# Kernel tuning notes

Measured on AMD Instinct MI355X. Metric: run time of the kernel, lower is better.

The kernel has to match this reference:

```python
import jax, jax.numpy as jnp
import numpy as np

B, N, C, H = 8, 1024, 768, 12
D = C // H
HID = 4 * C
MAX_TEXT_LEN = 512
LN_EPS = 1e-5


def _ln(x, g, b):
    mu = jnp.mean(x, axis=-1, keepdims=True)
    var = jnp.mean(jnp.square(x - mu), axis=-1, keepdims=True)
    return (x - mu) * jax.lax.rsqrt(var + LN_EPS) * g + b


def _mlp(x, w1, b1, w2, b2):
    h = jax.nn.gelu(x @ w1.T + b1, approximate=False)
    return h @ w2.T + b2


def setup_inputs() -> dict:
    key = jax.random.key(0)
    ks = jax.random.split(key, 16)
    s = 0.02
    return {
        "x": jax.random.normal(ks[0], (B, N, C), jnp.float32),
        "mask": jax.random.randint(ks[1], (B, N), 0, 2).astype(bool),
        "rel_bias": jax.random.normal(ks[2], (H, N, N), jnp.float32) * s,
        "w_qkv": jax.random.normal(ks[3], (3 * C, C), jnp.float32) * s,
        "q_bias": jnp.zeros((C,), jnp.float32),
        "v_bias": jnp.zeros((C,), jnp.float32),
        "w_proj": jax.random.normal(ks[4], (C, C), jnp.float32) * s,
        "b_proj": jnp.zeros((C,), jnp.float32),
        "ln1_g": jnp.ones((C,), jnp.float32),
        "ln1_b": jnp.zeros((C,), jnp.float32),
        "ln2t_g": jnp.ones((C,), jnp.float32),
        "ln2t_b": jnp.zeros((C,), jnp.float32),
        "ln2i_g": jnp.ones((C,), jnp.float32),
        "ln2i_b": jnp.zeros((C,), jnp.float32),
        "w1t": jax.random.normal(ks[5], (HID, C), jnp.float32) * s,
        "b1t": jnp.zeros((HID,), jnp.float32),
        "w2t": jax.random.normal(ks[6], (C, HID), jnp.float32) * s,
        "b2t": jnp.zeros((C,), jnp.float32),
        "w1i": jax.random.normal(ks[7], (HID, C), jnp.float32) * s,
        "b1i": jnp.zeros((HID,), jnp.float32),
        "w2i": jax.random.normal(ks[8], (C, HID), jnp.float32) * s,
        "b2i": jnp.zeros((C,), jnp.float32),
        "gamma1": jnp.full((C,), 0.1, jnp.float32),
        "gamma2": jnp.full((C,), 0.1, jnp.float32),
    }


def reference(x, mask, rel_bias, w_qkv, q_bias, v_bias, w_proj, b_proj,
              ln1_g, ln1_b, ln2t_g, ln2t_b, ln2i_g, ln2i_b,
              w1t, b1t, w2t, b2t, w1i, b1i, w2i, b2i, gamma1, gamma2):
    # ---- attention branch ----
    h = _ln(x, ln1_g, ln1_b)
    qkv_bias = jnp.concatenate([q_bias, jnp.zeros_like(v_bias), v_bias])
    qkv = h @ w_qkv.T + qkv_bias                      # [B,N,3C]
    qkv = qkv.reshape(B, N, 3, H, D).transpose(2, 0, 3, 1, 4)  # [3,B,H,N,D]
    q, k, v = qkv[0], qkv[1], qkv[2]
    q = q * (D ** -0.5)
    attn = jnp.einsum('bhnd,bhmd->bhnm',
                      q.astype(jnp.float32), k.astype(jnp.float32))
    attn = attn + rel_bias[None]                      # [B,H,N,N]
    attn = jnp.where(mask[:, None, None, :], attn, -jnp.inf)
    attn = jax.nn.softmax(attn, axis=-1).astype(x.dtype)
    out = jnp.einsum('bhnm,bhmd->bhnd', attn, v)
    out = out.transpose(0, 2, 1, 3).reshape(B, N, C)
    out = out @ w_proj.T + b_proj
    x = x + gamma1 * out
    # ---- dual-branch layer-scaled MLP (mlp_vl is None path) ----
    xt = x[:, :MAX_TEXT_LEN]
    xi = x[:, MAX_TEXT_LEN:]
    xt = xt + gamma2 * _mlp(_ln(xt, ln2t_g, ln2t_b), w1t, b1t, w2t, b2t)
    xi = xi + gamma2 * _mlp(_ln(xi, ln2i_g, ln2i_b), w1i, b1i, w2i, b2i)
    return jnp.concatenate([xt, xi], axis=1)
```

## Files before the change

### kernel.cpp

```cpp
#include <hip/hip_runtime.h>
#include <hip/hip_bf16.h>
#include <math.h>

#define B_    8
#define N_TOK 1024
#define C_    768
#define H_    12
#define D_    64
#define HID_  3072

typedef __attribute__((ext_vector_type(4)))  float f32x4;
typedef __attribute__((ext_vector_type(16))) float f32x16;
typedef __attribute__((ext_vector_type(8)))  short s16x8;
typedef __attribute__((ext_vector_type(4)))  unsigned short u16x4;

static __device__ __forceinline__ unsigned short f2bf(float x){
  union { __hip_bfloat16 h; unsigned short u; } cv;
  cv.h = __float2bfloat16(x);
  return cv.u;
}
static __device__ __forceinline__ float bf2f(unsigned short u){
  return __uint_as_float(((unsigned)u) << 16);
}

#define GLOAD_LDS16(gp, lp) \
  __builtin_amdgcn_global_load_lds((const __attribute__((address_space(1))) unsigned int*)(gp), \
                                   (__attribute__((address_space(3))) unsigned int*)(lp), 16, 0, 0)

__global__ __launch_bounds__(256) void k_cvtall(
    const float* __restrict__ wq,  const float* __restrict__ wp,
    const float* __restrict__ w1t, const float* __restrict__ w2t,
    const float* __restrict__ w1i, const float* __restrict__ w2i,
    const float* __restrict__ bias,
    unsigned short* __restrict__ dq,  unsigned short* __restrict__ dp,
    unsigned short* __restrict__ d1t, unsigned short* __restrict__ d2t,
    unsigned short* __restrict__ d1i, unsigned short* __restrict__ d2i,
    unsigned short* __restrict__ db)
{
  int i = blockIdx.x * 256 + threadIdx.x;
  const float* src; unsigned short* dst; int o;
  if      (i <  442368){ src = wq;  dst = dq;  o = i; }
  else if (i <  589824){ src = wp;  dst = dp;  o = i -  442368; }
  else if (i < 1179648){ src = w1t; dst = d1t; o = i -  589824; }
  else if (i < 1769472){ src = w2t; dst = d2t; o = i - 1179648; }
  else if (i < 2359296){ src = w1i; dst = d1i; o = i - 1769472; }
  else if (i < 2949120){ src = w2i; dst = d2i; o = i - 2359296; }
  else                 { src = bias;dst = db;  o = i - 2949120; }
  float4 v = ((const float4*)src)[o];
  u16x4 r;
  r.x = f2bf(v.x); r.y = f2bf(v.y); r.z = f2bf(v.z); r.w = f2bf(v.w);
  *(u16x4*)(dst + (size_t)o*4) = r;
}

__global__ __launch_bounds__(256) void k_ln1(const float* __restrict__ x,
                                             const float* __restrict__ g,
                                             const float* __restrict__ bta,
                                             unsigned short* __restrict__ out){
  int row  = blockIdx.x*4 + (threadIdx.x >> 6);
  int lane = threadIdx.x & 63;
  const float* xr = x + (size_t)row*C_;
  float v[12]; float s = 0.f;
  #pragma unroll
  for (int i=0;i<12;i++){ v[i] = xr[lane + i*64]; s += v[i]; }
  #pragma unroll
  for (int m=1;m<64;m<<=1) s += __shfl_xor(s, m);
  float mu = s * (1.f/768.f);
  float vs = 0.f;
  #pragma unroll
  for (int i=0;i<12;i++){ float d = v[i]-mu; vs += d*d; }
  #pragma unroll
  for (int m=1;m<64;m<<=1) vs += __shfl_xor(vs, m);
  float rs = rsqrtf(vs*(1.f/768.f) + 1e-5f);
  unsigned short* orow = out + (size_t)row*C_;
  #pragma unroll
  for (int i=0;i<12;i++){ int c = lane + i*64; orow[c] = f2bf((v[i]-mu)*rs*g[c] + bta[c]); }
}

__global__ __launch_bounds__(256) void k_ln2(const float* __restrict__ xmid,
                                             const float* __restrict__ gt, const float* __restrict__ bt,
                                             const float* __restrict__ gi, const float* __restrict__ bi,
                                             unsigned short* __restrict__ outc){
  int row  = blockIdx.x*4 + (threadIdx.x >> 6);
  int lane = threadIdx.x & 63;
  int bb = row >> 10, n = row & 1023;
  const float* G = (n < 512) ? gt : gi;
  const float* Bb = (n < 512) ? bt : bi;
  int crow = (n < 512) ? (bb*512 + n) : (4096 + bb*512 + (n - 512));
  const float* xr = xmid + (size_t)row*C_;
  float v[12]; float s = 0.f;
  #pragma unroll
  for (int i=0;i<12;i++){ v[i] = xr[lane + i*64]; s += v[i]; }
  #pragma unroll
  for (int m=1;m<64;m<<=1) s += __shfl_xor(s, m);
  float mu = s * (1.f/768.f);
  float vs = 0.f;
  #pragma unroll
  for (int i=0;i<12;i++){ float d = v[i]-mu; vs += d*d; }
  #pragma unroll
  for (int m=1;m<64;m<<=1) vs += __shfl_xor(vs, m);
  float rs = rsqrtf(vs*(1.f/768.f) + 1e-5f);
  unsigned short* orow = outc + (size_t)crow*C_;
  #pragma unroll
  for (int i=0;i<12;i++){ int c = lane + i*64; orow[c] = f2bf((v[i]-mu)*rs*G[c] + Bb[c]); }
}

template<int MODE>
__global__ __launch_bounds__(256, 3) void k_gemm2(
    const unsigned short* __restrict__ A,
    const unsigned short* __restrict__ Bw0,
    const unsigned short* __restrict__ Bw1,
    int K,
    const float* __restrict__ bias0,
    const float* __restrict__ bias1,
    const float* __restrict__ qb2,
    const float* __restrict__ resid,
    const float* __restrict__ gamma,
    unsigned short* __restrict__ out_bf,
    float* __restrict__ out_f)
{
  __shared__ __align__(16) char smem[49152];
  const int tid = threadIdx.x;
  const int lane = tid & 63, w = tid >> 6;
  const int wr = w >> 1, wc = w & 1;
  const int g16 = lane >> 4, c16 = lane & 15;

  const int gx = gridDim.x;
  const int nwg = gx * gridDim.y;
  const int flat = blockIdx.y * gx + blockIdx.x;
  const int nid = (flat & 7) * (nwg >> 3) + (flat >> 3);
  const int bx = nid % gx, by = nid / gx;
  const int z = blockIdx.z;
  const int row0 = bx*128, col0 = by*128;

  const unsigned short* Ap = A;
  const unsigned short* Bp = Bw0;
  const float* bias = bias0;
  if (MODE == 2 || MODE == 3){
    if (z){ Ap = A + (size_t)4096*K; Bp = Bw1; bias = bias1; }
  }
  const char* Abase = (const char*)Ap;
  const char* Bbase = (const char*)Bp;
  const size_t rowbytes = (size_t)K*2;
  const int KT2 = K >> 5;

  auto stage = [&](int h, int slot_idx){
    char* slot = smem + slot_idx*16384;
    size_t kb = (size_t)h*64;
    #pragma unroll
    for (int it = 0; it < 2; it++){
      int L = it*4096 + tid*16;
      int r = L >> 6, cb = L & 63;
      int scb = cb ^ ((r & 6) << 3);
      GLOAD_LDS16(Abase + (size_t)(row0 + r)*rowbytes + kb + scb, slot + L);
    }
    #pragma unroll
    for (int it = 0; it < 2; it++){
      int L = it*4096 + tid*16;
      int r = L >> 6, cb = L & 63;
      int scb = cb ^ ((r & 6) << 3);
      GLOAD_LDS16(Bbase + (size_t)(col0 + r)*rowbytes + kb + scb, slot + 8192 + L);
    }
  };

  stage(0, 0); stage(1, 1);
  asm volatile("s_waitcnt vmcnt(4)" ::: "memory");
  __builtin_amdgcn_s_barrier();

  f32x4 acc[4][4] = {};
  int sh = 2;
  int sc_ = 0;
  for (int h = 0; h < KT2; h++){
    if (h + 2 < KT2){
      stage(h + 2, sh);
      sh = (sh == 2) ? 0 : sh + 1;
    }
    char* slot = smem + sc_*16384;
    sc_ = (sc_ == 2) ? 0 : sc_ + 1;
    s16x8 af[4], bf[4];
    #pragma unroll
    for (int i = 0; i < 4; i++){
      int ra = wr*64 + i*16 + c16;
      af[i] = *(const s16x8*)(slot + ra*64 + ((g16*16) ^ ((ra & 6) << 3)));
      int rb = wc*64 + i*16 + c16;
      bf[i] = *(const s16x8*)(slot + 8192 + rb*64 + ((g16*16) ^ ((rb & 6) << 3)));
    }
    __builtin_amdgcn_s_setprio(1);
    #pragma unroll
    for (int mi = 0; mi < 4; mi++)
      #pragma unroll
      for (int ni = 0; ni < 4; ni++)
        acc[mi][ni] = __builtin_amdgcn_mfma_f32_16x16x32_bf16(af[mi], bf[ni], acc[mi][ni], 0, 0, 0);
    __builtin_amdgcn_s_setprio(0);
    if (h + 1 < KT2){
      if (h + 2 < KT2) asm volatile("s_waitcnt vmcnt(4)" ::: "memory");
      else             asm volatile("s_waitcnt vmcnt(0)" ::: "memory");
      __builtin_amdgcn_s_barrier();
    }
  }

  #pragma unroll
  for (int mi = 0; mi < 4; mi++){
    int mbase = row0 + wr*64 + mi*16 + g16*4;
    #pragma unroll
    for (int ni = 0; ni < 4; ni++){
      int j = col0 + wc*64 + ni*16 + c16;
      f32x4 a = acc[mi][ni];
      if (MODE == 0){
        int which = (j >= 1536) ? 2 : (j >= 768 ? 1 : 0);
        int cj = j - which*768;
        float bs = (which == 0) ? bias0[cj] : (which == 2 ? qb2[cj] : 0.f);
        int head = cj >> 6, d = cj & 63;
        #pragma unroll
        for (int r = 0; r < 4; r++){
          int mm = mbase + r;
          int bb = mm >> 10, n = mm & 1023;
          float val = a[r] + bs;
          if (which == 0) val *= 0.125f;
          out_bf[((((size_t)which*B_ + bb)*H_ + head)*N_TOK + n)*D_ + d] = f2bf(val);
        }
      } else if (MODE == 1){
        float gm = gamma[j], bs = bias[j];
        #pragma unroll
        for (int r = 0; r < 4; r++){
          size_t idx = (size_t)(mbase + r)*C_ + j;
          out_f[idx] = resid[idx] + gm*(a[r] + bs);
        }
      } else if (MODE == 2){
        float bs = bias[j];
        unsigned short* outp = out_bf + (size_t)z*4096*HID_;
        #pragma unroll
        for (int r = 0; r < 4; r++){
          float t = a[r] + bs;
          outp[(size_t)(mbase + r)*HID_ + j] = f2bf(0.5f*t*(1.f + erff(t*0.70710678118654752f)));
        }
      } else {
        float gm = gamma[j], bs = bias[j];
        #pragma unroll
        for (int r = 0; r < 4; r++){
          int mm = mbase + r;
          int bb = mm >> 9, n = (mm & 511) + (z ? 512 : 0);
          size_t idx = ((size_t)bb*N_TOK + n)*C_ + j;
          out_f[idx] = resid[idx] + gm*(a[r] + bs);
        }
      }
    }
  }
}

__global__ __launch_bounds__(256, 3) void k_attn(
    const unsigned short* __restrict__ qb,
    const unsigned short* __restrict__ kb,
    const unsigned short* __restrict__ vb,
    const unsigned short* __restrict__ bias_bf,
    const int* __restrict__ mask,
    unsigned short* __restrict__ outb)
{
  __shared__ __align__(16) char smem[45056];
  char* Vt0 = smem;
  char* Vt1 = smem + 8192;
  char* Ks  = smem + 16384;
  char* Bs  = smem + 24576;
  float* maskf = (float*)(smem + 40960);
  char* Oep = smem;

  int wg = blockIdx.x;
  int x = wg & 7, rest = wg >> 3;
  int qt = rest & 7, gl = rest >> 3;
  int g = gl*8 + x;
  int h = g % 12, bb = g / 12;

  const int tid = threadIdx.x, lane = tid & 63, w = tid >> 6;
  const int l31 = lane & 31, h5 = lane >> 5;
  const size_t bh = (size_t)bb*H_ + h;
  const char* qp = (const char*)(qb + bh*N_TOK*D_);
  const char* kp = (const char*)(kb + bh*N_TOK*D_);
  const unsigned short* vp = vb + bh*N_TOK*D_;
  const char* bp = (const char*)(bias_bf + (size_t)h*N_TOK*N_TOK);
  const int q0 = qt*128;
  const int qrow = q0 + w*32 + l31;
  const int qr = w*32 + l31;

  #pragma unroll
  for (int it = 0; it < 2; it++){
    int L = it*4096 + tid*16; int r = L >> 7, cb = L & 127;
    GLOAD_LDS16(kp + (size_t)r*128 + (cb ^ ((r & 7) << 4)), Ks + L);
  }
  #pragma unroll
  for (int it = 0; it < 4; it++){
    int L = it*4096 + tid*16; int r = L >> 7, cb = L & 127;
    GLOAD_LDS16(bp + (size_t)(q0 + r)*2048 + (cb ^ ((r & 7) << 4)), Bs + L);
  }
  unsigned short vv[16];
  #pragma unroll
  for (int j = 0; j < 16; j++) vv[j] = vp[(size_t)(w*16 + j)*D_ + lane];
  {
    int4 m4 = *(const int4*)(mask + bb*N_TOK + tid*4);
    float4 f4;
    f4.x = m4.x ? 0.f : -1e30f; f4.y = m4.y ? 0.f : -1e30f;
    f4.z = m4.z ? 0.f : -1e30f; f4.w = m4.w ? 0.f : -1e30f;
    *(float4*)(maskf + tid*4) = f4;
  }
  s16x8 qf[4];
  #pragma unroll
  for (int t = 0; t < 4; t++)
    qf[t] = *(const s16x8*)(qp + (size_t)qrow*128 + t*32 + h5*16);
  #pragma unroll
  for (int i = 0; i < 2; i++){
    s16x8 pk;
    #pragma unroll
    for (int e = 0; e < 8; e++) pk[e] = (short)vv[i*8 + e];
    *(s16x8*)(Vt0 + lane*128 + ((w*32 + i*16) ^ ((lane & 7) << 4))) = pk;
  }
  __syncthreads();

  f32x16 oacc[2] = {};
  float lrow = 0.f;

  for (int t = 0; t < 16; t++){
    const int kt = t*64;
    char* Vbuf = (t & 1) ? Vt1 : Vt0;
    char* Vnxt = (t & 1) ? Vt0 : Vt1;

    s16x8 kfr[2][4];
    #pragma unroll
    for (int ck = 0; ck < 2; ck++)
      #pragma unroll
      for (int tt = 0; tt < 4; tt++)
        kfr[ck][tt] = *(const s16x8*)(Ks + (ck*32 + l31)*128 + ((tt*32 + h5*16) ^ ((l31 & 7) << 4)));
    u16x4 bv[2][4];
    #pragma unroll
    for (int ck = 0; ck < 2; ck++)
      #pragma unroll
      for (int rq = 0; rq < 4; rq++){
        int off = ck*64 + rq*16 + h5*8;
        bv[ck][rq] = *(const u16x4*)(Bs + qr*128 + (off ^ ((qr & 7) << 4)));
      }
    __syncthreads();

    if (t < 15){
      #pragma unroll
      for (int it = 0; it < 2; it++){
        int L = it*4096 + tid*16; int r = L >> 7, cb = L & 127;
        GLOAD_LDS16(kp + (size_t)(kt + 64 + r)*128 + (cb ^ ((r & 7) << 4)), Ks + L);
      }
      #pragma unroll
      for (int it = 0; it < 4; it++){
        int L = it*4096 + tid*16; int r = L >> 7, cb = L & 127;
        GLOAD_LDS16(bp + (size_t)(q0 + r)*2048 + (size_t)(kt + 64)*2 + (cb ^ ((r & 7) << 4)), Bs + L);
      }
      #pragma unroll
      for (int j = 0; j < 16; j++)
        vv[j] = vp[(size_t)(kt + 64 + w*16 + j)*D_ + lane];
    }

    f32x16 sacc[2] = {};
    __builtin_amdgcn_s_setprio(1);
    #pragma unroll
    for (int tt = 0; tt < 4; tt++){
      sacc[0] = __builtin_amdgcn_mfma_f32_32x32x16_bf16(kfr[0][tt], qf[tt], sacc[0], 0, 0, 0);
      sacc[1] = __builtin_amdgcn_mfma_f32_32x32x16_bf16(kfr[1][tt], qf[tt], sacc[1], 0, 0, 0);
    }
    __builtin_amdgcn_s_setprio(0);

    float sv[2][16];
    float ps = 0.f;
    #pragma unroll
    for (int ck = 0; ck < 2; ck++){
      #pragma unroll
      for (int r = 0; r < 16; r++){
        int kk = ck*32 + (r & 3) + 8*(r >> 2) + 4*h5;
        float p = __expf(sacc[ck][r] + bf2f(bv[ck][r >> 2][r & 3]) + maskf[kt + kk]);
        sv[ck][r] = p;
        ps += p;
      }
    }
    lrow += ps;

    #pragma unroll
    for (int ck = 0; ck < 2; ck++){
      #pragma unroll
      for (int kh = 0; kh < 2; kh++){
        unsigned wA, wB, wC, wD;
        asm("v_cvt_pk_bf16_f32 %0, %1, %2" : "=v"(wA) : "v"(sv[ck][kh*8+0]), "v"(sv[ck][kh*8+1]));
        asm("v_cvt_pk_bf16_f32 %0, %1, %2" : "=v"(wB) : "v"(sv[ck][kh*8+2]), "v"(sv[ck][kh*8+3]));
        asm("v_cvt_pk_bf16_f32 %0, %1, %2" : "=v"(wC) : "v"(sv[ck][kh*8+4]), "v"(sv[ck][kh*8+5]));
        asm("v_cvt_pk_bf16_f32 %0, %1, %2" : "=v"(wD) : "v"(sv[ck][kh*8+6]), "v"(sv[ck][kh*8+7]));
        unsigned tA = (unsigned)__shfl_xor((int)wA, 32);
        unsigned tB = (unsigned)__shfl_xor((int)wB, 32);
        unsigned tC = (unsigned)__shfl_xor((int)wC, 32);
        unsigned tD = (unsigned)__shfl_xor((int)wD, 32);
        union { unsigned u[4]; s16x8 v; } pu;
        pu.u[0] = h5 ? tC : wA;
        pu.u[1] = h5 ? tD : wB;
        pu.u[2] = h5 ? wC : tA;
        pu.u[3] = h5 ? wD : tB;
        __builtin_amdgcn_s_setprio(1);
        #pragma unroll
        for (int dt = 0; dt < 2; dt++){
          int d = dt*32 + l31;
          s16x8 vf = *(const s16x8*)(Vbuf + d*128 + ((ck*64 + kh*32 + h5*16) ^ ((d & 7) << 4)));
          oacc[dt] = __builtin_amdgcn_mfma_f32_32x32x16_bf16(vf, pu.v, oacc[dt], 0, 0, 0);
        }
        __builtin_amdgcn_s_setprio(0);
      }
    }

    if (t < 15){
      #pragma unroll
      for (int i = 0; i < 2; i++){
        s16x8 pk;
        #pragma unroll
        for (int e = 0; e < 8; e++) pk[e] = (short)vv[i*8 + e];
        *(s16x8*)(Vnxt + lane*128 + ((w*32 + i*16) ^ ((lane & 7) << 4))) = pk;
      }
    }
    __syncthreads();
  }

  lrow += __shfl_xor(lrow, 32);
  float inv = 1.f / lrow;
  char* Ow = Oep + w*8192;
  #pragma unroll
  for (int dt = 0; dt < 2; dt++)
    #pragma unroll
    for (int r = 0; r < 16; r++){
      int d = dt*32 + (r & 3) + 8*(r >> 2) + 4*h5;
      *(float*)(Ow + l31*256 + ((d*4) ^ ((l31 & 7) << 4))) = oacc[dt][r] * inv;
    }
  int q2 = lane >> 1, dh = lane & 1;
  float of[32];
  #pragma unroll
  for (int i = 0; i < 8; i++){
    f32x4 v4 = *(const f32x4*)(Ow + q2*256 + ((dh*128 + i*16) ^ ((q2 & 7) << 4)));
    of[i*4+0] = v4[0]; of[i*4+1] = v4[1]; of[i*4+2] = v4[2]; of[i*4+3] = v4[3];
  }
  unsigned short* orow = outb + ((size_t)bb*N_TOK + q0 + w*32 + q2)*C_ + h*64 + dh*32;
  #pragma unroll
  for (int i = 0; i < 4; i++){
    s16x8 ob;
    #pragma unroll
    for (int e = 0; e < 8; e++) ob[e] = (short)f2bf(of[i*8+e]);
    *(s16x8*)(orow + i*8) = ob;
  }
}

extern "C" void kernel_launch(void* const* d_in, const int* in_sizes, int n_in,
                              void* d_out, int out_size, void* d_ws, size_t ws_size,
                              hipStream_t stream) {
  const float* x      = (const float*)d_in[0];
  const int*   mask   = (const int*)  d_in[1];
  const float* relb   = (const float*)d_in[2];
  const float* w_qkv  = (const float*)d_in[3];
  const float* q_bias = (const float*)d_in[4];
  const float* v_bias = (const float*)d_in[5];
  const float* w_proj = (const float*)d_in[6];
  const float* b_proj = (const float*)d_in[7];
  const float* ln1_g  = (const float*)d_in[8];
  const float* ln1_b  = (const float*)d_in[9];
  const float* ln2t_g = (const float*)d_in[10];
  const float* ln2t_b = (const float*)d_in[11];
  const float* ln2i_g = (const float*)d_in[12];
  const float* ln2i_b = (const float*)d_in[13];
  const float* w1t    = (const float*)d_in[14];
  const float* b1t    = (const float*)d_in[15];
  const float* w2t    = (const float*)d_in[16];
  const float* b2t    = (const float*)d_in[17];
  const float* w1i    = (const float*)d_in[18];
  const float* b1i    = (const float*)d_in[19];
  const float* w2i    = (const float*)d_in[20];
  const float* b2i    = (const float*)d_in[21];
  const float* gamma1 = (const float*)d_in[22];
  const float* gamma2 = (const float*)d_in[23];
  float* out = (float*)d_out;
  char* ws = (char*)d_ws;

  size_t off = 0;
  auto nxt = [&](size_t b){ size_t r = off; off += (b + 255) & ~(size_t)255; return r; };
  unsigned short* wq_bf  = (unsigned short*)(ws + nxt((size_t)3*C_*C_*2));
  unsigned short* wp_bf  = (unsigned short*)(ws + nxt((size_t)C_*C_*2));
  unsigned short* w1t_bf = (unsigned short*)(ws + nxt((size_t)HID_*C_*2));
  unsigned short* w2t_bf = (unsigned short*)(ws + nxt((size_t)HID_*C_*2));
  unsigned short* w1i_bf = (unsigned short*)(ws + nxt((size_t)HID_*C_*2));
  unsigned short* w2i_bf = (unsigned short*)(ws + nxt((size_t)HID_*C_*2));
  unsigned short* hln    = (unsigned short*)(ws + nxt((size_t)B_*N_TOK*C_*2));
  unsigned short* qkv    = (unsigned short*)(ws + nxt((size_t)3*B_*N_TOK*C_*2));
  unsigned short* attno  = (unsigned short*)(ws + nxt((size_t)B_*N_TOK*C_*2));
  float*          xmid   = (float*)(ws + nxt((size_t)B_*N_TOK*C_*4));
  unsigned short* ln2c   = hln;
  unsigned short* hidden = qkv;
  unsigned short* bias_bf = (unsigned short*)xmid;

  k_cvtall<<<dim3(23808), 256, 0, stream>>>(w_qkv, w_proj, w1t, w2t, w1i, w2i, relb,
                                            wq_bf, wp_bf, w1t_bf, w2t_bf, w1i_bf, w2i_bf, bias_bf);

  k_ln1<<<dim3(B_*N_TOK/4), 256, 0, stream>>>(x, ln1_g, ln1_b, hln);

  k_gemm2<0><<<dim3(64, 18, 1), 256, 0, stream>>>(hln, wq_bf, nullptr, C_,
                                                  q_bias, nullptr, v_bias,
                                                  nullptr, nullptr, qkv, nullptr);

  const size_t qsz = (size_t)B_*H_*N_TOK*D_;
  k_attn<<<dim3(768), 256, 0, stream>>>(qkv, qkv + qsz, qkv + 2*qsz, bias_bf, mask, attno);

  k_gemm2<1><<<dim3(64, 6, 1), 256, 0, stream>>>(attno, wp_bf, nullptr, C_,
                                                 b_proj, nullptr, nullptr,
                                                 x, gamma1, nullptr, xmid);

  k_ln2<<<dim3(B_*N_TOK/4), 256, 0, stream>>>(xmid, ln2t_g, ln2t_b, ln2i_g, ln2i_b, ln2c);

  k_gemm2<2><<<dim3(32, 24, 2), 256, 0, stream>>>(ln2c, w1t_bf, w1i_bf, C_,
                                                  b1t, b1i, nullptr,
                                                  nullptr, nullptr, hidden, nullptr);

  k_gemm2<3><<<dim3(32, 6, 2), 256, 0, stream>>>(hidden, w2t_bf, w2i_bf, HID_,
                                                 b2t, b2i, nullptr,
                                                 xmid, gamma2, nullptr, out);
}
```

Baseline: 322.4 us.

## Use 32x32 MFMA in GEMMs and read fp32 rel-bias directly in attention

```diff
diff --git a/kernel.cpp b/kernel.cpp
--- a/kernel.cpp
+++ b/kernel.cpp
@@ -19,9 +19,6 @@
   cv.h = __float2bfloat16(x);
   return cv.u;
 }
-static __device__ __forceinline__ float bf2f(unsigned short u){
-  return __uint_as_float(((unsigned)u) << 16);
-}
 
 #define GLOAD_LDS16(gp, lp) \
   __builtin_amdgcn_global_load_lds((const __attribute__((address_space(1))) unsigned int*)(gp), \
@@ -31,11 +28,9 @@
     const float* __restrict__ wq,  const float* __restrict__ wp,
     const float* __restrict__ w1t, const float* __restrict__ w2t,
     const float* __restrict__ w1i, const float* __restrict__ w2i,
-    const float* __restrict__ bias,
     unsigned short* __restrict__ dq,  unsigned short* __restrict__ dp,
     unsigned short* __restrict__ d1t, unsigned short* __restrict__ d2t,
-    unsigned short* __restrict__ d1i, unsigned short* __restrict__ d2i,
-    unsigned short* __restrict__ db)
+    unsigned short* __restrict__ d1i, unsigned short* __restrict__ d2i)
 {
   int i = blockIdx.x * 256 + threadIdx.x;
   const float* src; unsigned short* dst; int o;
@@ -44,8 +39,7 @@
   else if (i < 1179648){ src = w1t; dst = d1t; o = i -  589824; }
   else if (i < 1769472){ src = w2t; dst = d2t; o = i - 1179648; }
   else if (i < 2359296){ src = w1i; dst = d1i; o = i - 1769472; }
-  else if (i < 2949120){ src = w2i; dst = d2i; o = i - 2359296; }
-  else                 { src = bias;dst = db;  o = i - 2949120; }
+  else                 { src = w2i; dst = d2i; o = i - 2359296; }
   float4 v = ((const float4*)src)[o];
   u16x4 r;
   r.x = f2bf(v.x); r.y = f2bf(v.y); r.z = f2bf(v.z); r.w = f2bf(v.w);
@@ -122,7 +116,7 @@
   const int tid = threadIdx.x;
   const int lane = tid & 63, w = tid >> 6;
   const int wr = w >> 1, wc = w & 1;
-  const int g16 = lane >> 4, c16 = lane & 15;
+  const int l31 = lane & 31, h5 = lane >> 5;
 
   const int gx = gridDim.x;
   const int nwg = gx * gridDim.y;
@@ -166,7 +160,7 @@
   asm volatile("s_waitcnt vmcnt(4)" ::: "memory");
   __builtin_amdgcn_s_barrier();
 
-  f32x4 acc[4][4] = {};
+  f32x16 acc[2][2] = {};
   int sh = 2;
   int sc_ = 0;
   for (int h = 0; h < KT2; h++){
@@ -176,20 +170,29 @@
     }
     char* slot = smem + sc_*16384;
     sc_ = (sc_ == 2) ? 0 : sc_ + 1;
-    s16x8 af[4], bf[4];
-    #pragma unroll
-    for (int i = 0; i < 4; i++){
-      int ra = wr*64 + i*16 + c16;
-      af[i] = *(const s16x8*)(slot + ra*64 + ((g16*16) ^ ((ra & 6) << 3)));
-      int rb = wc*64 + i*16 + c16;
-      bf[i] = *(const s16x8*)(slot + 8192 + rb*64 + ((g16*16) ^ ((rb & 6) << 3)));
+    s16x8 af[2][2], bfr[2][2];
+    #pragma unroll
+    for (int fm = 0; fm < 2; fm++){
+      int ra = wr*64 + fm*32 + l31;
+      int swa = (ra & 6) << 3;
+      af[fm][0] = *(const s16x8*)(slot + ra*64 + ((h5*16) ^ swa));
+      af[fm][1] = *(const s16x8*)(slot + ra*64 + ((32 + h5*16) ^ swa));
+    }
+    #pragma unroll
+    for (int fn = 0; fn < 2; fn++){
+      int rb = wc*64 + fn*32 + l31;
+      int swb = (rb & 6) << 3;
+      bfr[fn][0] = *(const s16x8*)(slot + 8192 + rb*64 + ((h5*16) ^ swb));
+      bfr[fn][1] = *(const s16x8*)(slot + 8192 + rb*64 + ((32 + h5*16) ^ swb));
     }
     __builtin_amdgcn_s_setprio(1);
     #pragma unroll
-    for (int mi = 0; mi < 4; mi++)
-      #pragma unroll
-      for (int ni = 0; ni < 4; ni++)
-        acc[mi][ni] = __builtin_amdgcn_mfma_f32_16x16x32_bf16(af[mi], bf[ni], acc[mi][ni], 0, 0, 0);
+    for (int kh = 0; kh < 2; kh++)
+      #pragma unroll
+      for (int fm = 0; fm < 2; fm++)
+        #pragma unroll
+        for (int fn = 0; fn < 2; fn++)
+          acc[fm][fn] = __builtin_amdgcn_mfma_f32_32x32x16_bf16(af[fm][kh], bfr[fn][kh], acc[fm][fn], 0, 0, 0);
     __builtin_amdgcn_s_setprio(0);
     if (h + 1 < KT2){
       if (h + 2 < KT2) asm volatile("s_waitcnt vmcnt(4)" ::: "memory");
@@ -198,47 +201,49 @@
     }
   }
 
-  #pragma unroll
-  for (int mi = 0; mi < 4; mi++){
-    int mbase = row0 + wr*64 + mi*16 + g16*4;
-    #pragma unroll
-    for (int ni = 0; ni < 4; ni++){
-      int j = col0 + wc*64 + ni*16 + c16;
-      f32x4 a = acc[mi][ni];
+  const float QSCALE = 0.18033688011f;
+  #pragma unroll
+  for (int fm = 0; fm < 2; fm++){
+    #pragma unroll
+    for (int fn = 0; fn < 2; fn++){
+      int j = col0 + wc*64 + fn*32 + l31;
+      f32x16 a = acc[fm][fn];
       if (MODE == 0){
         int which = (j >= 1536) ? 2 : (j >= 768 ? 1 : 0);
         int cj = j - which*768;
         float bs = (which == 0) ? bias0[cj] : (which == 2 ? qb2[cj] : 0.f);
         int head = cj >> 6, d = cj & 63;
         #pragma unroll
-        for (int r = 0; r < 4; r++){
-          int mm = mbase + r;
-          int bb = mm >> 10, n = mm & 1023;
+        for (int r = 0; r < 16; r++){
+          int m = row0 + wr*64 + fm*32 + (r & 3) + 8*(r >> 2) + 4*h5;
+          int bb = m >> 10, n = m & 1023;
           float val = a[r] + bs;
-          if (which == 0) val *= 0.125f;
+          if (which == 0) val *= QSCALE;
           out_bf[((((size_t)which*B_ + bb)*H_ + head)*N_TOK + n)*D_ + d] = f2bf(val);
         }
       } else if (MODE == 1){
         float gm = gamma[j], bs = bias[j];
         #pragma unroll
-        for (int r = 0; r < 4; r++){
-          size_t idx = (size_t)(mbase + r)*C_ + j;
+        for (int r = 0; r < 16; r++){
+          int m = row0 + wr*64 + fm*32 + (r & 3) + 8*(r >> 2) + 4*h5;
+          size_t idx = (size_t)m*C_ + j;
           out_f[idx] = resid[idx] + gm*(a[r] + bs);
         }
       } else if (MODE == 2){
         float bs = bias[j];
         unsigned short* outp = out_bf + (size_t)z*4096*HID_;
         #pragma unroll
-        for (int r = 0; r < 4; r++){
+        for (int r = 0; r < 16; r++){
+          int m = row0 + wr*64 + fm*32 + (r & 3) + 8*(r >> 2) + 4*h5;
           float t = a[r] + bs;
-          outp[(size_t)(mbase + r)*HID_ + j] = f2bf(0.5f*t*(1.f + erff(t*0.70710678118654752f)));
+          outp[(size_t)m*HID_ + j] = f2bf(0.5f*t*(1.f + erff(t*0.70710678118654752f)));
         }
       } else {
         float gm = gamma[j], bs = bias[j];
         #pragma unroll
-        for (int r = 0; r < 4; r++){
-          int mm = mbase + r;
-          int bb = mm >> 9, n = (mm & 511) + (z ? 512 : 0);
+        for (int r = 0; r < 16; r++){
+          int m = row0 + wr*64 + fm*32 + (r & 3) + 8*(r >> 2) + 4*h5;
+          int bb = m >> 9, n = (m & 511) + (z ? 512 : 0);
           size_t idx = ((size_t)bb*N_TOK + n)*C_ + j;
           out_f[idx] = resid[idx] + gm*(a[r] + bs);
         }
@@ -247,20 +252,20 @@
   }
 }
 
-__global__ __launch_bounds__(256, 3) void k_attn(
+__global__ __launch_bounds__(256, 2) void k_attn(
     const unsigned short* __restrict__ qb,
     const unsigned short* __restrict__ kb,
     const unsigned short* __restrict__ vb,
-    const unsigned short* __restrict__ bias_bf,
+    const float* __restrict__ relb,
     const int* __restrict__ mask,
     unsigned short* __restrict__ outb)
 {
-  __shared__ __align__(16) char smem[45056];
+  __shared__ __align__(16) char smem[61440];
   char* Vt0 = smem;
   char* Vt1 = smem + 8192;
   char* Ks  = smem + 16384;
   char* Bs  = smem + 24576;
-  float* maskf = (float*)(smem + 40960);
+  float* maskf = (float*)(smem + 57344);
   char* Oep = smem;
 
   int wg = blockIdx.x;
@@ -275,7 +280,7 @@
   const char* qp = (const char*)(qb + bh*N_TOK*D_);
   const char* kp = (const char*)(kb + bh*N_TOK*D_);
   const unsigned short* vp = vb + bh*N_TOK*D_;
-  const char* bp = (const char*)(bias_bf + (size_t)h*N_TOK*N_TOK);
+  const char* bp = (const char*)(relb + (size_t)h*N_TOK*N_TOK);
   const int q0 = qt*128;
   const int qrow = q0 + w*32 + l31;
   const int qr = w*32 + l31;
@@ -286,9 +291,9 @@
     GLOAD_LDS16(kp + (size_t)r*128 + (cb ^ ((r & 7) << 4)), Ks + L);
   }
   #pragma unroll
-  for (int it = 0; it < 4; it++){
-    int L = it*4096 + tid*16; int r = L >> 7, cb = L & 127;
-    GLOAD_LDS16(bp + (size_t)(q0 + r)*2048 + (cb ^ ((r & 7) << 4)), Bs + L);
+  for (int it = 0; it < 8; it++){
+    int L = it*4096 + tid*16; int r = L >> 8, cb = L & 255;
+    GLOAD_LDS16(bp + (size_t)(q0 + r)*4096 + (cb ^ ((r & 15) << 4)), Bs + L);
   }
   unsigned short vv[16];
   #pragma unroll
@@ -327,13 +332,13 @@
       #pragma unroll
       for (int tt = 0; tt < 4; tt++)
         kfr[ck][tt] = *(const s16x8*)(Ks + (ck*32 + l31)*128 + ((tt*32 + h5*16) ^ ((l31 & 7) << 4)));
-    u16x4 bv[2][4];
+    f32x4 bvf[2][4];
     #pragma unroll
     for (int ck = 0; ck < 2; ck++)
       #pragma unroll
       for (int rq = 0; rq < 4; rq++){
-        int off = ck*64 + rq*16 + h5*8;
-        bv[ck][rq] = *(const u16x4*)(Bs + qr*128 + (off ^ ((qr & 7) << 4)));
+        int off = ck*128 + rq*32 + h5*16;
+        bvf[ck][rq] = *(const f32x4*)(Bs + qr*256 + (off ^ ((qr & 15) << 4)));
       }
     __syncthreads();
 
@@ -344,9 +349,9 @@
         GLOAD_LDS16(kp + (size_t)(kt + 64 + r)*128 + (cb ^ ((r & 7) << 4)), Ks + L);
       }
       #pragma unroll
-      for (int it = 0; it < 4; it++){
-        int L = it*4096 + tid*16; int r = L >> 7, cb = L & 127;
-        GLOAD_LDS16(bp + (size_t)(q0 + r)*2048 + (size_t)(kt + 64)*2 + (cb ^ ((r & 7) << 4)), Bs + L);
+      for (int it = 0; it < 8; it++){
+        int L = it*4096 + tid*16; int r = L >> 8, cb = L & 255;
+        GLOAD_LDS16(bp + (size_t)(q0 + r)*4096 + (size_t)(kt + 64)*4 + (cb ^ ((r & 15) << 4)), Bs + L);
       }
       #pragma unroll
       for (int j = 0; j < 16; j++)
@@ -369,7 +374,8 @@
       #pragma unroll
       for (int r = 0; r < 16; r++){
         int kk = ck*32 + (r & 3) + 8*(r >> 2) + 4*h5;
-        float p = __expf(sacc[ck][r] + bf2f(bv[ck][r >> 2][r & 3]) + maskf[kt + kk]);
+        float p = exp2f(fmaf(bvf[ck][r >> 2][r & 3], 1.44269504089f,
+                             sacc[ck][r] + maskf[kt + kk]));
         sv[ck][r] = p;
         ps += p;
       }
@@ -488,10 +494,9 @@
   float*          xmid   = (float*)(ws + nxt((size_t)B_*N_TOK*C_*4));
   unsigned short* ln2c   = hln;
   unsigned short* hidden = qkv;
-  unsigned short* bias_bf = (unsigned short*)xmid;
-
-  k_cvtall<<<dim3(23808), 256, 0, stream>>>(w_qkv, w_proj, w1t, w2t, w1i, w2i, relb,
-                                            wq_bf, wp_bf, w1t_bf, w2t_bf, w1i_bf, w2i_bf, bias_bf);
+
+  k_cvtall<<<dim3(11520), 256, 0, stream>>>(w_qkv, w_proj, w1t, w2t, w1i, w2i,
+                                            wq_bf, wp_bf, w1t_bf, w2t_bf, w1i_bf, w2i_bf);
 
   k_ln1<<<dim3(B_*N_TOK/4), 256, 0, stream>>>(x, ln1_g, ln1_b, hln);
 
@@ -500,7 +505,7 @@
                                                   nullptr, nullptr, qkv, nullptr);
 
   const size_t qsz = (size_t)B_*H_*N_TOK*D_;
-  k_attn<<<dim3(768), 256, 0, stream>>>(qkv, qkv + qsz, qkv + 2*qsz, bias_bf, mask, attno);
+  k_attn<<<dim3(768), 256, 0, stream>>>(qkv, qkv + qsz, qkv + 2*qsz, relb, mask, attno);
 
   k_gemm2<1><<<dim3(64, 6, 1), 256, 0, stream>>>(attno, wp_bf, nullptr, C_,
                                                  b_proj, nullptr, nullptr,
```

Result: no change. 322.3 us (-0.0%).
